# Performance work log

Hardware: AMD Instinct MI355X
Metric: run time of the kernel (lower is better)

The kernel has to match this reference:

```python
import jax, jax.numpy as jnp
import numpy as np

N = 50000
E = 1600000
DIM = 128
RC = 5.0
DEPTH = 3


def setup_inputs() -> dict:
    key = jax.random.key(0)
    kv, ke, ks, kd, kw, kb, krs, ksig = jax.random.split(key, 8)
    v = jax.random.normal(kv, (N, DIM), dtype=jnp.float32)
    # edge distances in [0, rc]
    e = jax.random.uniform(ke, (E, 1), dtype=jnp.float32) * RC
    src = jax.random.randint(ks, (E,), 0, N, dtype=jnp.int32)
    dst = jax.random.randint(kd, (E,), 0, N, dtype=jnp.int32)
    # learned params: A = nn.Linear(dim, dim); rs, sigma = torch.rand(1)
    A_w = jax.random.normal(kw, (DIM, DIM), dtype=jnp.float32) / np.sqrt(DIM)
    A_b = jax.random.normal(kb, (DIM,), dtype=jnp.float32) * 0.01
    rs = jax.random.uniform(krs, (1,), dtype=jnp.float32)
    sigma = jax.random.uniform(ksig, (1,), dtype=jnp.float32)
    return {"v": v, "e": e, "src": src, "dst": dst,
            "A_w": A_w, "A_b": A_b, "rs": rs, "sigma": sigma}


def _edge_envelope(r, rs, sigma):
    # exp(-(r-rs)^2/sigma^2) * 0.5 * cos(pi*r/rc) * (r < rc)
    gauss = jnp.exp(-jnp.square(r - rs) / jnp.square(sigma))
    cutoff = 0.5 * jnp.cos(np.pi * r / RC) * (r < RC).astype(r.dtype)
    return gauss * cutoff


def reference(v, e, src, dst, A_w, A_b, rs, sigma):
    f = _edge_envelope(e, rs, sigma)  # [E, 1]
    cur = v
    for _ in range(DEPTH):
        msg = f * cur[src]  # gather src node feats, weight by edge envelope: [E, DIM]
        svf = jax.ops.segment_sum(msg, dst, num_segments=N)  # scatter-sum to dst: [N, DIM]
        cur = jax.nn.relu((svf + v) @ A_w.T + A_b)  # linear + relu, skip from original v
    return cur
```

## Files before the change

kernel.cpp:

```cpp
#include <hip/hip_runtime.h>
#include <math.h>

#define N_NODES 50000
#define N_PAD   50048
#define N_EDGES 1600000
#define DIM     128
#define RCUT    5.0f
#define NGROUP  (N_PAD / 64)
#define NB_PRE  256
#define CH_PRE  (N_EDGES / NB_PRE)
#define NB_CONV 6250
#define NB_WPREP 8

typedef __attribute__((ext_vector_type(8))) __bf16 bf16x8;
typedef __attribute__((ext_vector_type(4))) float  f32x4;

__device__ __forceinline__ float bf_lo(unsigned int u) { return __uint_as_float(u << 16); }
__device__ __forceinline__ float bf_hi(unsigned int u) { return __uint_as_float(u & 0xffff0000u); }
__device__ __forceinline__ unsigned short f2bf(float x) {
    unsigned int u = __float_as_uint(x);
    u += 0x7fffu + ((u >> 16) & 1u);
    return (unsigned short)(u >> 16);
}

__global__ __launch_bounds__(256) void preA_kernel(
        const float* __restrict__ v, unsigned short* __restrict__ vb,
        const float* __restrict__ Aw, uint4* __restrict__ wfrag,
        const int* __restrict__ dst, int* __restrict__ partial) {
    int b = blockIdx.x;
    if (b < NB_CONV) {
        int i = b * 256 + threadIdx.x;
        float4 x = ((const float4*)v)[i];
        uint2 o;
        o.x = (unsigned)f2bf(x.x) | ((unsigned)f2bf(x.y) << 16);
        o.y = (unsigned)f2bf(x.z) | ((unsigned)f2bf(x.w) << 16);
        ((uint2*)vb)[i] = o;
    } else if (b < NB_CONV + NB_WPREP) {
        int t = (b - NB_CONV) * 256 + threadIdx.x;
        int lane = t & 63, nt = (t >> 6) & 7, kk = t >> 9;
        int n  = nt * 16 + (lane & 15);
        int k0 = kk * 32 + (lane >> 4) * 8;
        unsigned short h[8];
        #pragma unroll
        for (int i = 0; i < 8; ++i) h[i] = f2bf(Aw[n * DIM + k0 + i]);
        uint4 o;
        o.x = h[0] | ((unsigned)h[1] << 16); o.y = h[2] | ((unsigned)h[3] << 16);
        o.z = h[4] | ((unsigned)h[5] << 16); o.w = h[6] | ((unsigned)h[7] << 16);
        wfrag[t] = o;
    } else {
        __shared__ int h[NGROUP];
        int cb = b - NB_CONV - NB_WPREP, tid = threadIdx.x;
        for (int g = tid; g < NGROUP; g += 256) h[g] = 0;
        __syncthreads();
        int beg = cb * CH_PRE, end = beg + CH_PRE;
        for (int i = beg + tid; i < end; i += 256)
            atomicAdd(&h[dst[i] >> 6], 1);
        __syncthreads();
        for (int g = tid; g < NGROUP; g += 256) partial[cb * NGROUP + g] = h[g];
    }
}

__global__ __launch_bounds__(1024) void preB_kernel(
        const int* __restrict__ partial,
        int* __restrict__ goff,
        int* __restrict__ pbase) {
    __shared__ int part[1024];
    int tid = threadIdx.x;
    int s = 0;
    if (tid < NGROUP)
        for (int b = 0; b < NB_PRE; ++b) s += partial[b * NGROUP + tid];
    part[tid] = (tid < NGROUP) ? s : 0;
    __syncthreads();
    for (int d = 1; d < 1024; d <<= 1) {
        int val = (tid >= d) ? part[tid - d] : 0;
        __syncthreads(); part[tid] += val; __syncthreads();
    }
    int base = (tid == 0) ? 0 : part[tid - 1];
    if (tid < NGROUP) {
        goff[tid] = base;
        int run = base;
        for (int b = 0; b < NB_PRE; ++b) {
            pbase[b * NGROUP + tid] = run;
            run += partial[b * NGROUP + tid];
        }
    }
    if (tid == 0) goff[NGROUP] = N_EDGES;
}

__global__ __launch_bounds__(256) void reorder_kernel(
        const float* __restrict__ e,
        const int*   __restrict__ src,
        const int*   __restrict__ dst,
        const float* __restrict__ rs,
        const float* __restrict__ sigma,
        const int*   __restrict__ pbase,
        int2* __restrict__ metaT) {
    __shared__ int base[NGROUP];
    __shared__ int cnt[NGROUP];
    int b = blockIdx.x, tid = threadIdx.x;
    for (int g = tid; g < NGROUP; g += 256) { base[g] = pbase[b * NGROUP + g]; cnt[g] = 0; }
    __syncthreads();
    float rsv = rs[0], sg = sigma[0];
    int beg = b * CH_PRE, end = beg + CH_PRE;
    for (int i = beg + tid; i < end; i += 256) {
        float r  = e[i];
        float d  = r - rsv;
        float gauss = expf(-(d * d) / (sg * sg));
        float cut   = 0.5f * cosf(r * (float)(M_PI / (double)RCUT));
        cut = (r < RCUT) ? cut : 0.0f;
        float fe = gauss * cut;
        int dn = dst[i];
        int g  = dn >> 6;
        int lr = atomicAdd(&cnt[g], 1);
        metaT[base[g] + lr] = make_int2(src[i] * (DIM * 2) | ((dn & 63) << 24),
                                        __float_as_int(fe));
    }
}

__global__ __launch_bounds__(256) void tagsort_kernel(
        const int2* __restrict__ metaT,
        const int*  __restrict__ goff,
        int2* __restrict__ meta,
        int*  __restrict__ off) {
    __shared__ int cnt[64], base[64], cur[64];
    int g = blockIdx.x, tid = threadIdx.x;
    int sbeg = goff[g], send = goff[g + 1];
    if (tid < 64) cnt[tid] = 0;
    __syncthreads();
    for (int i = sbeg + tid; i < send; i += 256)
        atomicAdd(&cnt[(metaT[i].x >> 24) & 63], 1);
    __syncthreads();
    if (tid == 0) {
        int run = 0;
        #pragma unroll
        for (int t = 0; t < 64; ++t) { base[t] = run; cur[t] = run; run += cnt[t]; }
    }
    __syncthreads();
    if (tid < 64) {
        int node = g * 64 + tid;
        if (node <= N_NODES) off[node] = sbeg + base[tid];
    }
    __syncthreads();
    for (int i = sbeg + tid; i < send; i += 256) {
        int2 m = metaT[i];
        int tag = (m.x >> 24) & 63;
        int lr = atomicAdd(&cur[tag], 1);
        meta[sbeg + lr] = make_int2(m.x & 0x00FFFFFF, m.y);
    }
}

#define EDGE2(mx, mf, rr)                                        \
    do {                                                         \
        float ff = __int_as_float(mf);                           \
        a0 = fmaf(ff, bf_lo(rr), a0);                            \
        a1 = fmaf(ff, bf_hi(rr), a1);                            \
    } while (0)

__global__ __launch_bounds__(256) void gather_kernel(
        const unsigned short* __restrict__ cur,
        const float* __restrict__ v,
        const int2*  __restrict__ meta,
        const int*   __restrict__ off,
        unsigned short* __restrict__ svf) {
    int n    = (blockIdx.x << 2) + (threadIdx.x >> 6);
    int lane = threadIdx.x & 63;

    float2 vv = *(const float2*)(v + (size_t)n * DIM + lane * 2);
    float a0 = vv.x, a1 = vv.y;

    int beg = __builtin_amdgcn_readfirstlane(off[n]);
    int end = __builtin_amdgcn_readfirstlane(off[n + 1]);
    const char* base = (const char*)cur + lane * 4;

    int c = beg;
    if ((c & 1) && c < end) {
        int2 m = meta[c];
        unsigned rr = *(const unsigned*)(base + (unsigned)m.x);
        EDGE2(m.x, m.y, rr);
        ++c;
    }
    for (; c + 16 <= end; c += 16) {
        int4 m0 = *(const int4*)(meta + c);
        int4 m1 = *(const int4*)(meta + c + 2);
        int4 m2 = *(const int4*)(meta + c + 4);
        int4 m3 = *(const int4*)(meta + c + 6);
        int4 m4 = *(const int4*)(meta + c + 8);
        int4 m5 = *(const int4*)(meta + c + 10);
        int4 m6 = *(const int4*)(meta + c + 12);
        int4 m7 = *(const int4*)(meta + c + 14);
        unsigned r0  = *(const unsigned*)(base + (unsigned)m0.x);
        unsigned r1  = *(const unsigned*)(base + (unsigned)m0.z);
        unsigned r2  = *(const unsigned*)(base + (unsigned)m1.x);
        unsigned r3  = *(const unsigned*)(base + (unsigned)m1.z);
        unsigned r4  = *(const unsigned*)(base + (unsigned)m2.x);
        unsigned r5  = *(const unsigned*)(base + (unsigned)m2.z);
        unsigned r6  = *(const unsigned*)(base + (unsigned)m3.x);
        unsigned r7  = *(const unsigned*)(base + (unsigned)m3.z);
        unsigned r8  = *(const unsigned*)(base + (unsigned)m4.x);
        unsigned r9  = *(const unsigned*)(base + (unsigned)m4.z);
        unsigned r10 = *(const unsigned*)(base + (unsigned)m5.x);
        unsigned r11 = *(const unsigned*)(base + (unsigned)m5.z);
        unsigned r12 = *(const unsigned*)(base + (unsigned)m6.x);
        unsigned r13 = *(const unsigned*)(base + (unsigned)m6.z);
        unsigned r14 = *(const unsigned*)(base + (unsigned)m7.x);
        unsigned r15 = *(const unsigned*)(base + (unsigned)m7.z);
        EDGE2(m0.x, m0.y, r0);  EDGE2(m0.z, m0.w, r1);
        EDGE2(m1.x, m1.y, r2);  EDGE2(m1.z, m1.w, r3);
        EDGE2(m2.x, m2.y, r4);  EDGE2(m2.z, m2.w, r5);
        EDGE2(m3.x, m3.y, r6);  EDGE2(m3.z, m3.w, r7);
        EDGE2(m4.x, m4.y, r8);  EDGE2(m4.z, m4.w, r9);
        EDGE2(m5.x, m5.y, r10); EDGE2(m5.z, m5.w, r11);
        EDGE2(m6.x, m6.y, r12); EDGE2(m6.z, m6.w, r13);
        EDGE2(m7.x, m7.y, r14); EDGE2(m7.z, m7.w, r15);
    }
    if (c + 8 <= end) {
        int4 m0 = *(const int4*)(meta + c);
        int4 m1 = *(const int4*)(meta + c + 2);
        int4 m2 = *(const int4*)(meta + c + 4);
        int4 m3 = *(const int4*)(meta + c + 6);
        unsigned r0 = *(const unsigned*)(base + (unsigned)m0.x);
        unsigned r1 = *(const unsigned*)(base + (unsigned)m0.z);
        unsigned r2 = *(const unsigned*)(base + (unsigned)m1.x);
        unsigned r3 = *(const unsigned*)(base + (unsigned)m1.z);
        unsigned r4 = *(const unsigned*)(base + (unsigned)m2.x);
        unsigned r5 = *(const unsigned*)(base + (unsigned)m2.z);
        unsigned r6 = *(const unsigned*)(base + (unsigned)m3.x);
        unsigned r7 = *(const unsigned*)(base + (unsigned)m3.z);
        EDGE2(m0.x, m0.y, r0); EDGE2(m0.z, m0.w, r1);
        EDGE2(m1.x, m1.y, r2); EDGE2(m1.z, m1.w, r3);
        EDGE2(m2.x, m2.y, r4); EDGE2(m2.z, m2.w, r5);
        EDGE2(m3.x, m3.y, r6); EDGE2(m3.z, m3.w, r7);
        c += 8;
    }
    for (; c < end; ++c) {
        int2 m = meta[c];
        unsigned rr = *(const unsigned*)(base + (unsigned)m.x);
        EDGE2(m.x, m.y, rr);
    }
    unsigned o = (unsigned)f2bf(a0) | ((unsigned)f2bf(a1) << 16);
    *(unsigned*)(svf + (size_t)n * DIM + lane * 2) = o;
}

__global__ __launch_bounds__(256) void gemm_kernel(
        const unsigned short* __restrict__ X,
        const uint4* __restrict__ wfrag,
        const float* __restrict__ bias,
        unsigned short* __restrict__ out_bf,
        float* __restrict__ out_f,
        int last) {
    __shared__ uint4 wlds[2048];
    int tid = threadIdx.x;
    for (int i = tid; i < 2048; i += 256) wlds[i] = wfrag[i];

    int wv = tid >> 6, lane = tid & 63;
    int quad = lane >> 4, l16 = lane & 15;
    int row = blockIdx.x * 64 + wv * 16 + l16;

    f32x4 acc[8];
    #pragma unroll
    for (int i = 0; i < 8; ++i) acc[i] = (f32x4){0.f, 0.f, 0.f, 0.f};

    __syncthreads();

    const unsigned short* xp = X + (size_t)row * DIM + quad * 8;
    #pragma unroll
    for (int kk = 0; kk < 4; ++kk) {
        bf16x8 af = *(const bf16x8*)(xp + kk * 32);
        #pragma unroll
        for (int nt = 0; nt < 8; ++nt) {
            uint4 w = wlds[(kk * 8 + nt) * 64 + lane];
            bf16x8 bfr = __builtin_bit_cast(bf16x8, w);
            acc[nt] = __builtin_amdgcn_mfma_f32_16x16x32_bf16(af, bfr, acc[nt], 0, 0, 0);
        }
    }

    int orow0 = blockIdx.x * 64 + wv * 16 + quad * 4;
    #pragma unroll
    for (int nt = 0; nt < 8; ++nt) {
        int col = nt * 16 + l16;
        float b = bias[col];
        #pragma unroll
        for (int r = 0; r < 4; ++r) {
            int orow = orow0 + r;
            if (orow < N_NODES) {
                float val = fmaxf(acc[nt][r] + b, 0.f);
                if (last) out_f[(size_t)orow * DIM + col] = val;
                else      out_bf[(size_t)orow * DIM + col] = f2bf(val);
            }
        }
    }
}

extern "C" void kernel_launch(void* const* d_in, const int* in_sizes, int n_in,
                              void* d_out, int out_size, void* d_ws, size_t ws_size,
                              hipStream_t stream) {
    const float* v     = (const float*)d_in[0];
    const float* e     = (const float*)d_in[1];
    const int*   src   = (const int*)  d_in[2];
    const int*   dst   = (const int*)  d_in[3];
    const float* Aw    = (const float*)d_in[4];
    const float* Ab    = (const float*)d_in[5];
    const float* rs    = (const float*)d_in[6];
    const float* sigma = (const float*)d_in[7];
    float* out = (float*)d_out;

    char* p = (char*)d_ws;
    int2*           meta  = (int2*)p;            p += (size_t)N_EDGES * 8;
    unsigned short* bufV  = (unsigned short*)p;  p += (size_t)N_PAD * DIM * 2;
    unsigned short* bufA  = (unsigned short*)p;  p += (size_t)N_PAD * DIM * 2;
    unsigned short* bufB  = (unsigned short*)p;  p += (size_t)N_PAD * DIM * 2;
    uint4*          wfrag = (uint4*)p;           p += 2048 * 16;
    int*            off   = (int*)p;             p += (size_t)(N_NODES + 1) * 4;
    int*            goff  = (int*)p;             p += (NGROUP + 2) * 4;
    int2* metaT   = (int2*)bufA;
    int*  partial = (int*)bufB;
    int*  pbase   = partial + NB_PRE * NGROUP;

    preA_kernel<<<NB_CONV + NB_WPREP + NB_PRE, 256, 0, stream>>>(
        v, bufV, Aw, wfrag, dst, partial);
    preB_kernel<<<1, 1024, 0, stream>>>(partial, goff, pbase);
    reorder_kernel<<<NB_PRE, 256, 0, stream>>>(e, src, dst, rs, sigma, pbase, metaT);
    tagsort_kernel<<<NGROUP, 256, 0, stream>>>(metaT, goff, meta, off);

    const int GB = N_NODES / 4;
    const int MB = N_PAD / 64;

    gather_kernel<<<GB, 256, 0, stream>>>(bufV, v, meta, off, bufA);
    gemm_kernel<<<MB, 256, 0, stream>>>(bufA, wfrag, Ab, bufB, nullptr, 0);
    gather_kernel<<<GB, 256, 0, stream>>>(bufB, v, meta, off, bufA);
    gemm_kernel<<<MB, 256, 0, stream>>>(bufA, wfrag, Ab, bufV, nullptr, 0);
    gather_kernel<<<GB, 256, 0, stream>>>(bufV, v, meta, off, bufA);
    gemm_kernel<<<MB, 256, 0, stream>>>(bufA, wfrag, Ab, nullptr, out, 1);
}
```

Baseline: 362.8 us.

## Parallelize bucket scan, double reorder blocks, read bf16 skip input in gather

Replaces the single-block serial preB kernel with three kernels: a parallel column sum, a small scan, and a parallel per-group base computation. The number of pre-sort partitions doubles and reorder blocks grow to 512 threads. The gather kernel now reads the bf16 copy of v for its skip term instead of fp32, and keeps bufV intact by ping-ponging between bufA and bufB. This cuts the serial prefix work and the gather's memory traffic, but adds kernel launches and bf16 rounding of the skip input.

```diff
diff --git a/kernel.cpp b/kernel.cpp
--- a/kernel.cpp
+++ b/kernel.cpp
@@ -7,7 +7,7 @@
 #define DIM     128
 #define RCUT    5.0f
 #define NGROUP  (N_PAD / 64)
-#define NB_PRE  256
+#define NB_PRE  512
 #define CH_PRE  (N_EDGES / NB_PRE)
 #define NB_CONV 6250
 #define NB_WPREP 8
@@ -60,34 +60,50 @@
     }
 }
 
-__global__ __launch_bounds__(1024) void preB_kernel(
-        const int* __restrict__ partial,
-        int* __restrict__ goff,
-        int* __restrict__ pbase) {
-    __shared__ int part[1024];
+__global__ __launch_bounds__(256) void ktot_kernel(const int* __restrict__ partial,
+                                                   int* __restrict__ gtot) {
+    int g = blockIdx.x * 256 + threadIdx.x;
+    if (g >= NGROUP) return;
+    int s = 0;
+    for (int b = 0; b < NB_PRE; ++b) s += partial[b * NGROUP + g];
+    gtot[g] = s;
+}
+
+__global__ __launch_bounds__(256) void kscan_kernel(const int* __restrict__ gtot,
+                                                    int* __restrict__ goff) {
+    __shared__ int part[256];
     int tid = threadIdx.x;
-    int s = 0;
-    if (tid < NGROUP)
-        for (int b = 0; b < NB_PRE; ++b) s += partial[b * NGROUP + tid];
-    part[tid] = (tid < NGROUP) ? s : 0;
-    __syncthreads();
-    for (int d = 1; d < 1024; d <<= 1) {
+    int i0 = tid * 4;
+    int v[4]; int s = 0;
+    #pragma unroll
+    for (int k = 0; k < 4; ++k) { int i = i0 + k; v[k] = (i < NGROUP) ? gtot[i] : 0; s += v[k]; }
+    part[tid] = s; __syncthreads();
+    for (int d = 1; d < 256; d <<= 1) {
         int val = (tid >= d) ? part[tid - d] : 0;
         __syncthreads(); part[tid] += val; __syncthreads();
     }
-    int base = (tid == 0) ? 0 : part[tid - 1];
-    if (tid < NGROUP) {
-        goff[tid] = base;
-        int run = base;
-        for (int b = 0; b < NB_PRE; ++b) {
-            pbase[b * NGROUP + tid] = run;
-            run += partial[b * NGROUP + tid];
-        }
+    int run = (tid == 0) ? 0 : part[tid - 1];
+    #pragma unroll
+    for (int k = 0; k < 4; ++k) {
+        int i = i0 + k;
+        if (i < NGROUP) { goff[i] = run; run += v[k]; }
     }
     if (tid == 0) goff[NGROUP] = N_EDGES;
 }
 
-__global__ __launch_bounds__(256) void reorder_kernel(
+__global__ __launch_bounds__(256) void kbase_kernel(const int* __restrict__ partial,
+                                                    const int* __restrict__ goff,
+                                                    int* __restrict__ pbase) {
+    int g = blockIdx.x * 256 + threadIdx.x;
+    if (g >= NGROUP) return;
+    int run = goff[g];
+    for (int b = 0; b < NB_PRE; ++b) {
+        pbase[b * NGROUP + g] = run;
+        run += partial[b * NGROUP + g];
+    }
+}
+
+__global__ __launch_bounds__(512) void reorder_kernel(
         const float* __restrict__ e,
         const int*   __restrict__ src,
         const int*   __restrict__ dst,
@@ -98,11 +114,11 @@
     __shared__ int base[NGROUP];
     __shared__ int cnt[NGROUP];
     int b = blockIdx.x, tid = threadIdx.x;
-    for (int g = tid; g < NGROUP; g += 256) { base[g] = pbase[b * NGROUP + g]; cnt[g] = 0; }
+    for (int g = tid; g < NGROUP; g += 512) { base[g] = pbase[b * NGROUP + g]; cnt[g] = 0; }
     __syncthreads();
     float rsv = rs[0], sg = sigma[0];
     int beg = b * CH_PRE, end = beg + CH_PRE;
-    for (int i = beg + tid; i < end; i += 256) {
+    for (int i = beg + tid; i < end; i += 512) {
         float r  = e[i];
         float d  = r - rsv;
         float gauss = expf(-(d * d) / (sg * sg));
@@ -158,15 +174,15 @@
 
 __global__ __launch_bounds__(256) void gather_kernel(
         const unsigned short* __restrict__ cur,
-        const float* __restrict__ v,
+        const unsigned short* __restrict__ vb,
         const int2*  __restrict__ meta,
         const int*   __restrict__ off,
         unsigned short* __restrict__ svf) {
     int n    = (blockIdx.x << 2) + (threadIdx.x >> 6);
     int lane = threadIdx.x & 63;
 
-    float2 vv = *(const float2*)(v + (size_t)n * DIM + lane * 2);
-    float a0 = vv.x, a1 = vv.y;
+    unsigned vv = *(const unsigned*)((const char*)vb + (size_t)n * (DIM * 2) + lane * 4);
+    float a0 = bf_lo(vv), a1 = bf_hi(vv);
 
     int beg = __builtin_amdgcn_readfirstlane(off[n]);
     int end = __builtin_amdgcn_readfirstlane(off[n + 1]);
@@ -311,6 +327,7 @@
     unsigned short* bufB  = (unsigned short*)p;  p += (size_t)N_PAD * DIM * 2;
     uint4*          wfrag = (uint4*)p;           p += 2048 * 16;
     int*            off   = (int*)p;             p += (size_t)(N_NODES + 1) * 4;
+    int*            gtot  = (int*)p;             p += (NGROUP + 2) * 4;
     int*            goff  = (int*)p;             p += (NGROUP + 2) * 4;
     int2* metaT   = (int2*)bufA;
     int*  partial = (int*)bufB;
@@ -318,17 +335,19 @@
 
     preA_kernel<<<NB_CONV + NB_WPREP + NB_PRE, 256, 0, stream>>>(
         v, bufV, Aw, wfrag, dst, partial);
-    preB_kernel<<<1, 1024, 0, stream>>>(partial, goff, pbase);
-    reorder_kernel<<<NB_PRE, 256, 0, stream>>>(e, src, dst, rs, sigma, pbase, metaT);
+    ktot_kernel<<<(NGROUP + 255) / 256, 256, 0, stream>>>(partial, gtot);
+    kscan_kernel<<<1, 256, 0, stream>>>(gtot, goff);
+    kbase_kernel<<<(NGROUP + 255) / 256, 256, 0, stream>>>(partial, goff, pbase);
+    reorder_kernel<<<NB_PRE, 512, 0, stream>>>(e, src, dst, rs, sigma, pbase, metaT);
     tagsort_kernel<<<NGROUP, 256, 0, stream>>>(metaT, goff, meta, off);
 
     const int GB = N_NODES / 4;
     const int MB = N_PAD / 64;
 
-    gather_kernel<<<GB, 256, 0, stream>>>(bufV, v, meta, off, bufA);
+    gather_kernel<<<GB, 256, 0, stream>>>(bufV, bufV, meta, off, bufA);
     gemm_kernel<<<MB, 256, 0, stream>>>(bufA, wfrag, Ab, bufB, nullptr, 0);
-    gather_kernel<<<GB, 256, 0, stream>>>(bufB, v, meta, off, bufA);
-    gemm_kernel<<<MB, 256, 0, stream>>>(bufA, wfrag, Ab, bufV, nullptr, 0);
-    gather_kernel<<<GB, 256, 0, stream>>>(bufV, v, meta, off, bufA);
+    gather_kernel<<<GB, 256, 0, stream>>>(bufB, bufV, meta, off, bufA);
+    gemm_kernel<<<MB, 256, 0, stream>>>(bufA, wfrag, Ab, bufB, nullptr, 0);
+    gather_kernel<<<GB, 256, 0, stream>>>(bufB, bufV, meta, off, bufA);
     gemm_kernel<<<MB, 256, 0, stream>>>(bufA, wfrag, Ab, nullptr, out, 1);
 }
```

Result: no change. 355.7 us (-1.9%).
